# Kernel tuning notes

Measured on AMD Instinct MI355X. Metric: run time of the kernel, lower is better.

## Reference

```python
import jax, jax.numpy as jnp
import numpy as np

HIDDEN = 2048
H = 16            # num heads
Q_RANK = 1536
KV_RANK = 512
D_NOPE = 128
D_ROPE = 64
D_QK = D_NOPE + D_ROPE   # 192
D_V = 128
ROPE_BASE = 10000.0
EPS = 1e-6


def _rms_norm(x, w):
    xf = x.astype(jnp.float32)
    var = jnp.mean(xf * xf, axis=-1, keepdims=True)
    return w * (xf * jax.lax.rsqrt(var + EPS)).astype(x.dtype)


def _rotate_half(x):
    x1, x2 = x[..., : x.shape[-1] // 2], x[..., x.shape[-1] // 2:]
    return jnp.concatenate((-x2, x1), axis=-1)


def _rope_cos_sin(position_ids, dtype):
    inv_freq = 1.0 / (ROPE_BASE ** (jnp.arange(0, D_ROPE, 2, dtype=jnp.float32) / D_ROPE))
    freqs = position_ids.astype(jnp.float32)[..., None] * inv_freq  # [b,s,32]
    emb = jnp.concatenate((freqs, freqs), axis=-1)                  # [b,s,64]
    return jnp.cos(emb).astype(dtype), jnp.sin(emb).astype(dtype)


def setup_inputs() -> dict:
    key = jax.random.key(0)
    ks = jax.random.split(key, 8)
    b, s = 1, 2048
    scale = 0.02
    return {
        "hidden_states": jax.random.normal(ks[0], (b, s, HIDDEN), jnp.float32),
        "position_ids": jnp.broadcast_to(jnp.arange(s, dtype=jnp.int64)[None, :], (b, s)),
        "q_a_w": jax.random.normal(ks[1], (Q_RANK, HIDDEN), jnp.float32) * scale,
        "q_a_ln_w": jnp.ones((Q_RANK,), jnp.float32),
        "q_b_w": jax.random.normal(ks[2], (H * D_QK, Q_RANK), jnp.float32) * scale,
        "kv_a_w": jax.random.normal(ks[3], (KV_RANK + D_ROPE, HIDDEN), jnp.float32) * scale,
        "kv_a_ln_w": jnp.ones((KV_RANK,), jnp.float32),
        "kv_b_w": jax.random.normal(ks[4], (H * (D_NOPE + D_V), KV_RANK), jnp.float32) * scale,
        "o_w": jax.random.normal(ks[5], (HIDDEN, H * D_V), jnp.float32) * scale,
    }


def reference(hidden_states, position_ids, q_a_w, q_a_ln_w, q_b_w, kv_a_w, kv_a_ln_w, kv_b_w, o_w):
    b, s, _ = hidden_states.shape
    softmax_scale = D_QK ** (-0.5)

    # Q path: low-rank down-proj -> RMSNorm -> up-proj
    q_a = hidden_states @ q_a_w.T                              # [b,s,q_rank]
    q = (_rms_norm(q_a, q_a_ln_w) @ q_b_w.T).reshape(b, s, H, D_QK)
    q_nope, q_pe = q[..., :D_NOPE], q[..., D_NOPE:]

    # KV path: joint down-proj -> split latent / rope part
    kv_a = hidden_states @ kv_a_w.T                            # [b,s,kv_rank+rope]
    compressed_kv = _rms_norm(kv_a[..., :KV_RANK], kv_a_ln_w)  # [b,s,kv_rank]
    k_pe = kv_a[..., KV_RANK:]                                 # [b,s,rope]
    kv_b = (compressed_kv @ kv_b_w.T).reshape(b, s, H, D_NOPE + D_V)
    k_nope, v = kv_b[..., :D_NOPE], kv_b[..., D_NOPE:]

    # decoupled RoPE on the rope slice
    cos, sin = _rope_cos_sin(position_ids, hidden_states.dtype)  # [b,s,64]
    cos, sin = cos[:, :, None, :], sin[:, :, None, :]            # [b,s,1,64]
    q_pe = q_pe * cos + _rotate_half(q_pe) * sin                 # [b,s,H,64]
    k_pe_h = jnp.broadcast_to(k_pe[:, :, None, :], (b, s, H, D_ROPE))
    k_pe_h = k_pe_h * cos + _rotate_half(k_pe_h) * sin

    q_full = jnp.concatenate([q_nope, q_pe], axis=-1)            # [b,s,H,192]
    k_full = jnp.concatenate([k_nope, k_pe_h], axis=-1)          # [b,s,H,192]

    # naive materialized attention (matches reference)
    scores = jnp.einsum("bqhd,bkhd->bhqk", q_full, k_full) * softmax_scale
    causal = jnp.triu(jnp.full((s, s), -jnp.inf, dtype=scores.dtype), k=1)
    scores = scores + causal
    probs = jax.nn.softmax(scores.astype(jnp.float32), axis=-1).astype(q_full.dtype)
    attn = jnp.einsum("bhqk,bkhd->bqhd", probs, v).reshape(b, s, H * D_V)
    return attn @ o_w.T
```

## Files before the change

### kernel.cpp

```cpp
#include <hip/hip_runtime.h>
#include <stdint.h>

#define S_LEN 2048
#define HIDDEN_ 2048
#define NH 16
#define QR 1536
#define KVR 512
#define DN 128
#define DR 64
#define DQK 192
#define DV 128
#define NQKV 2112

#define KT_STRIDE 6144
#define VT_STRIDE 4096

typedef __attribute__((ext_vector_type(8))) short bf16x8;
typedef __attribute__((ext_vector_type(4))) float f32x4;
typedef __attribute__((ext_vector_type(4))) unsigned short u16x4;
typedef unsigned short u16;
typedef unsigned int u32;

#define GLOAD_LDS16(g, l)                                                      \
    __builtin_amdgcn_global_load_lds(                                          \
        (const __attribute__((address_space(1))) void*)(g),                    \
        (__attribute__((address_space(3))) void*)(l), 16, 0, 0)

__device__ inline float bf2f(u16 x) {
    union { u32 u; float f; } v; v.u = ((u32)x) << 16; return v.f;
}
__device__ inline u16 f2bf(float f) {
    union { float f; u32 u; } v; v.f = f;
    u32 u = v.u;
    return (u16)((u + 0x7fffu + ((u >> 16) & 1u)) >> 16);
}

__global__ void cvt_multi(const float* s0, u16* d0, int n0,
                          const float* s1, u16* d1, int n1,
                          const float* s2, u16* d2, int n2,
                          const float* s3, u16* d3, int n3,
                          const float* s4, u16* d4, int n4,
                          const float* s5, u16* d5, int n5)
{
    const float* src; u16* dst; int n;
    switch (blockIdx.y) {
        case 0: src = s0; dst = d0; n = n0; break;
        case 1: src = s1; dst = d1; n = n1; break;
        case 2: src = s2; dst = d2; n = n2; break;
        case 3: src = s3; dst = d3; n = n3; break;
        case 4: src = s4; dst = d4; n = n4; break;
        default: src = s5; dst = d5; n = n5; break;
    }
    int i = (blockIdx.x * 256 + threadIdx.x) * 4;
    if (i + 3 < n) {
        float4 v = *(const float4*)(src + i);
        u16x4 o;
        o[0] = f2bf(v.x); o[1] = f2bf(v.y); o[2] = f2bf(v.z); o[3] = f2bf(v.w);
        *(u16x4*)(dst + i) = o;
    }
}

__device__ __forceinline__
void gemm_body(const u16* __restrict__ A, const u16* __restrict__ B,
               void* __restrict__ Cv, int M, int N, int Kloop, int ld,
               int out_f32, int bx, int by)
{
    __shared__ u16 sA[128 * 32];
    __shared__ u16 sB[128 * 32];
    const int tid  = threadIdx.x;
    const int wave = tid >> 6;
    const int lane = tid & 63;
    const int l16  = lane & 15;
    const int quad = lane >> 4;
    const int m_blk = by * 128;
    const int n_blk = bx * 128;
    const int wm = (wave >> 1) * 64;
    const int wn = (wave & 1) * 64;

    const f32x4 zero4 = {0.f, 0.f, 0.f, 0.f};
    f32x4 acc[4][4];
#pragma unroll
    for (int i = 0; i < 4; i++)
#pragma unroll
        for (int j = 0; j < 4; j++) acc[i][j] = zero4;

    const int srow = lane >> 2;
    const int scol = (lane & 3) * 8;

    for (int k0 = 0; k0 < Kloop; k0 += 32) {
        __syncthreads();
#pragma unroll
        for (int p = 0; p < 2; p++) {
            const int rbase = wave * 32 + p * 16;
            const int row = rbase + srow;
            const u16* ga = A + (size_t)(m_blk + row) * ld + k0 + scol;
            GLOAD_LDS16(ga, &sA[rbase * 32]);
            int brow = n_blk + row; if (brow >= N) brow = N - 1;
            const u16* gb = B + (size_t)brow * ld + k0 + scol;
            GLOAD_LDS16(gb, &sB[rbase * 32]);
        }
        __syncthreads();

        bf16x8 af[4], bfr[4];
#pragma unroll
        for (int i = 0; i < 4; i++)
            af[i] = *(const bf16x8*)(sA + (wm + i * 16 + l16) * 32 + quad * 8);
#pragma unroll
        for (int j = 0; j < 4; j++)
            bfr[j] = *(const bf16x8*)(sB + (wn + j * 16 + l16) * 32 + quad * 8);
#pragma unroll
        for (int i = 0; i < 4; i++)
#pragma unroll
            for (int j = 0; j < 4; j++)
                acc[i][j] = __builtin_amdgcn_mfma_f32_16x16x32_bf16(
                    af[i], bfr[j], acc[i][j], 0, 0, 0);
    }

#pragma unroll
    for (int i = 0; i < 4; i++)
#pragma unroll
        for (int j = 0; j < 4; j++)
#pragma unroll
            for (int r = 0; r < 4; r++) {
                int mrow = m_blk + wm + i * 16 + quad * 4 + r;
                int ncol = n_blk + wn + j * 16 + l16;
                if (ncol < N) {
                    if (out_f32)
                        ((float*)Cv)[(size_t)mrow * N + ncol] = acc[i][j][r];
                    else
                        ((u16*)Cv)[(size_t)mrow * N + ncol] = f2bf(acc[i][j][r]);
                }
            }
}

__global__ __launch_bounds__(256, 3)
void gemm_splitk(const u16* __restrict__ A, const u16* __restrict__ B,
                 float* __restrict__ C0, float* __restrict__ C1,
                 int M, int N, int Kh, int ld)
{
    float* C = blockIdx.z ? C1 : C0;
    gemm_body(A + (size_t)blockIdx.z * Kh, B + (size_t)blockIdx.z * Kh,
              C, M, N, Kh, ld, 1, blockIdx.x, blockIdx.y);
}

__global__ __launch_bounds__(256, 3)
void gemm_dual(const u16* A0, const u16* B0, u16* C0, int M0, int N0, int K0,
               const u16* A1, const u16* B1, u16* C1, int M1, int N1, int K1)
{
    if (blockIdx.z == 0) {
        if ((int)blockIdx.x >= (N0 + 127) / 128) return;
        gemm_body(A0, B0, C0, M0, N0, K0, K0, 0, blockIdx.x, blockIdx.y);
    } else {
        gemm_body(A1, B1, C1, M1, N1, K1, K1, 0, blockIdx.x, blockIdx.y);
    }
}

__global__ void rmsnorm2_k(const float* __restrict__ P0, const float* __restrict__ P1,
                           const float* __restrict__ W0, u16* __restrict__ Y0,
                           const float* __restrict__ W1, u16* __restrict__ Y1,
                           u16* __restrict__ kpe)
{
    const int row = blockIdx.x;
    const float* p0 = P0 + (size_t)row * NQKV;
    const float* p1 = P1 + (size_t)row * NQKV;
    __shared__ float xbuf[QR];
    __shared__ float red[4];
    int off, len; const float* W; u16* Y;
    if (blockIdx.y == 0) { off = 0;  len = QR;  W = W0; Y = Y0 + (size_t)row * QR;  }
    else                 { off = QR; len = KVR; W = W1; Y = Y1 + (size_t)row * KVR; }
    float ss = 0.f;
    for (int i = threadIdx.x; i < len; i += 256) {
        float v = p0[off + i] + p1[off + i];
        xbuf[i] = v;
        ss += v * v;
    }
#pragma unroll
    for (int o = 32; o; o >>= 1) ss += __shfl_down(ss, o, 64);
    if ((threadIdx.x & 63) == 0) red[threadIdx.x >> 6] = ss;
    __syncthreads();
    float tot = red[0] + red[1] + red[2] + red[3];
    float inv = 1.0f / sqrtf(tot / (float)len + 1e-6f);
    for (int i = threadIdx.x; i < len; i += 256)
        Y[i] = f2bf(W[i] * xbuf[i] * inv);
    if (blockIdx.y == 1 && threadIdx.x < DR) {
        int i = threadIdx.x;
        kpe[(size_t)row * DR + i] = f2bf(p0[QR + KVR + i] + p1[QR + KVR + i]);
    }
}

__global__ void rope_repack(const u16* __restrict__ q,
                            const u16* __restrict__ kvb,
                            const u16* __restrict__ kpe_b,
                            u16* __restrict__ Q, u16* __restrict__ Kf)
{
    const int s = blockIdx.x;
    const float pos = (float)s;
    const int t = threadIdx.x;
    __shared__ float cs[64], sn[64];
    __shared__ u16 kpe_r[64];
    if (t < 64) {
        int jf = t & 31;
        float freq = powf(10000.f, -(float)(2 * jf) / 64.f);
        float ang = pos * freq;
        cs[t] = cosf(ang);
        sn[t] = sinf(ang);
    }
    __syncthreads();
    if (t < 64) {
        int j = t;
        float x = bf2f(kpe_b[(size_t)s * DR + j]);
        float other = (j < 32) ? -bf2f(kpe_b[(size_t)s * DR + j + 32])
                               :  bf2f(kpe_b[(size_t)s * DR + j - 32]);
        kpe_r[j] = f2bf(x * cs[j] + other * sn[j]);
    }
    __syncthreads();

    for (int idx = t; idx < NH * 24; idx += 256) {
        const int h  = idx / 24;
        const int cg = idx % 24;
        const int d0v = cg * 8;
        const size_t qbase = (size_t)s * (NH * DQK) + h * DQK;
        bf16x8 qv, kv;
        if (d0v < DN) {
            qv = *(const bf16x8*)(q + qbase + d0v);
            kv = *(const bf16x8*)(kvb + (size_t)s * (NH * 256) + h * 256 + d0v);
        } else {
            const int j0 = d0v - DN;
#pragma unroll
            for (int e = 0; e < 8; e++) {
                int j = j0 + e;
                float x = bf2f(q[qbase + DN + j]);
                float other = (j < 32) ? -bf2f(q[qbase + DN + j + 32])
                                       :  bf2f(q[qbase + DN + j - 32]);
                qv[e] = (short)f2bf(x * cs[j] + other * sn[j]);
                kv[e] = (short)kpe_r[j];
            }
        }
        *(bf16x8*)&Q[((size_t)h * S_LEN + s) * DQK + d0v] = qv;
        const size_t koff = (size_t)(h * 64 + (s >> 5)) * KT_STRIDE
                          + (size_t)(cg * 32 + (s & 31)) * 8;
        *(bf16x8*)&Kf[koff] = kv;
    }
}

__global__ void transpose_v(const u16* __restrict__ kvb, u16* __restrict__ Vt)
{
    __shared__ u16 tile[64][72];
    const int h  = blockIdx.z;
    const int s0 = blockIdx.x * 64;
    const int d0 = blockIdx.y * 64;
    const int t  = threadIdx.x;
#pragma unroll
    for (int p = 0; p < 2; p++) {
        int c = p * 256 + t;
        int r = c >> 3, col = (c & 7) * 8;
        *(bf16x8*)&tile[r][col] =
            *(const bf16x8*)&kvb[(size_t)(s0 + r) * (NH * 256) + h * 256 + 128 + d0 + col];
    }
    __syncthreads();
#pragma unroll
    for (int p = 0; p < 2; p++) {
        int c = p * 256 + t;
        int dr = c >> 3, sc = (c & 7) * 8;
        bf16x8 v;
#pragma unroll
        for (int j = 0; j < 8; j++) v[j] = (short)tile[sc + j][dr];
        const int s_abs   = s0 + sc;
        const int kt      = s_abs >> 5;
        const int schunk  = (s_abs & 31) >> 3;
        const size_t voff = (size_t)(h * 64 + kt) * VT_STRIDE
                          + (size_t)(schunk * 128 + (d0 + dr)) * 8;
        *(bf16x8*)&Vt[voff] = v;
    }
}

__global__ __launch_bounds__(256, 3)
void mla_attn(const u16* __restrict__ Q, const u16* __restrict__ Kf,
              const u16* __restrict__ Vt, u16* __restrict__ attn,
              float* __restrict__ part)
{
    const int lin = blockIdx.x + 48 * blockIdx.y;
    const int h   = ((lin & 7) << 1) | ((lin >> 3) & 1);
    const int bx  = lin >> 4;

    int s, tb, te, cIdx; bool direct;
    if (bx < 16)      { s = 16 + bx; tb = 0;  te = 32;        cIdx = 0; direct = false; }
    else if (bx < 32) { s = 47 - bx; tb = 32; te = 2 * s + 2; cIdx = 1; direct = false; }
    else              { s = 47 - bx; tb = 0;  te = 2 * s + 2; cIdx = 0; direct = true;  }

    const int wave  = threadIdx.x >> 6;
    const int lane  = threadIdx.x & 63;
    const int l16   = lane & 15;
    const int quad  = lane >> 4;
    const int q0    = s * 64 + wave * 16;
    const int qrow  = q0 + l16;

    const u16* Qh  = Q  + (size_t)h * S_LEN * DQK;
    const u16* Kh  = Kf + (size_t)h * 64 * KT_STRIDE;
    const u16* Vth = Vt + (size_t)h * 64 * VT_STRIDE;

    __shared__ u16 sK[2][24 * 32 * 8];
    __shared__ u16 sV[2][4 * 128 * 8];
    __shared__ u16 pbuf[4][16][36];
    u16 (*pb)[36] = pbuf[wave];

    bf16x8 qf[6];
#pragma unroll
    for (int st = 0; st < 6; st++)
        qf[st] = *(const bf16x8*)(Qh + (size_t)qrow * DQK + st * 32 + quad * 8);

    const f32x4 zero4 = {0.f, 0.f, 0.f, 0.f};
    f32x4 oacc[8];
#pragma unroll
    for (int t = 0; t < 8; t++) oacc[t] = zero4;
    float mrow = -INFINITY, lrow = 0.f;

    const float scale = 0.07216878364870323f;

    auto stage = [&](int buf, int kt) {
        const u16* kp = Kh + (size_t)kt * KT_STRIDE;
#pragma unroll
        for (int g = 0; g < 3; g++)
            GLOAD_LDS16(kp + (g * 256 + wave * 64 + lane) * 8,
                        &sK[buf][(g * 256 + wave * 64) * 8]);
        const u16* vp = Vth + (size_t)kt * VT_STRIDE;
#pragma unroll
        for (int g = 0; g < 2; g++)
            GLOAD_LDS16(vp + (g * 256 + wave * 64 + lane) * 8,
                        &sV[buf][(g * 256 + wave * 64) * 8]);
    };

    stage(0, tb);

    for (int kt = tb; kt < te; kt++) {
        const int c0  = kt * 32;
        const int cur = (kt - tb) & 1;
        __syncthreads();
        if (kt + 1 < te) stage(cur ^ 1, kt + 1);

        if (c0 <= q0 + 15) {
            f32x4 s0 = zero4, s1 = zero4;
            __builtin_amdgcn_s_setprio(1);
#pragma unroll
            for (int st = 0; st < 6; st++) {
                bf16x8 k0 = *(const bf16x8*)&sK[cur][((st * 4 + quad) * 32 + l16) * 8];
                bf16x8 k1 = *(const bf16x8*)&sK[cur][((st * 4 + quad) * 32 + 16 + l16) * 8];
                s0 = __builtin_amdgcn_mfma_f32_16x16x32_bf16(k0, qf[st], s0, 0, 0, 0);
                s1 = __builtin_amdgcn_mfma_f32_16x16x32_bf16(k1, qf[st], s1, 0, 0, 0);
            }
            __builtin_amdgcn_s_setprio(0);
            bf16x8 vfr[8];
#pragma unroll
            for (int t = 0; t < 8; t++)
                vfr[t] = *(const bf16x8*)&sV[cur][(quad * 128 + t * 16 + l16) * 8];

            const bool full = (c0 + 31 <= q0);
            float v0[4], v1[4];
#pragma unroll
            for (int r = 0; r < 4; r++) {
                v0[r] = s0[r] * scale;
                v1[r] = s1[r] * scale;
                if (!full) {
                    if (c0 + quad * 4 + r > qrow)      v0[r] = -INFINITY;
                    if (c0 + 16 + quad * 4 + r > qrow) v1[r] = -INFINITY;
                }
            }
            float lm = fmaxf(fmaxf(fmaxf(v0[0], v0[1]), fmaxf(v0[2], v0[3])),
                             fmaxf(fmaxf(v1[0], v1[1]), fmaxf(v1[2], v1[3])));
            lm = fmaxf(lm, __shfl_xor(lm, 16, 64));
            lm = fmaxf(lm, __shfl_xor(lm, 32, 64));

            float mref;
            if (__all(lm <= mrow + 8.f)) {
                mref = mrow;
            } else {
                mref = fmaxf(mrow, lm);
                const float alpha = __expf(mrow - mref);
#pragma unroll
                for (int t = 0; t < 8; t++) oacc[t] *= alpha;
                lrow *= alpha;
                mrow = mref;
            }

            float p0[4], p1[4], rs = 0.f;
#pragma unroll
            for (int r = 0; r < 4; r++) {
                p0[r] = __expf(v0[r] - mref);
                p1[r] = __expf(v1[r] - mref);
                rs += p0[r] + p1[r];
            }
            rs += __shfl_xor(rs, 16, 64);
            rs += __shfl_xor(rs, 32, 64);
            lrow += rs;

            u16x4 pk0, pk1;
#pragma unroll
            for (int r = 0; r < 4; r++) { pk0[r] = f2bf(p0[r]); pk1[r] = f2bf(p1[r]); }
            *(u16x4*)&pb[l16][quad * 4]      = pk0;
            *(u16x4*)&pb[l16][16 + quad * 4] = pk1;
            asm volatile("s_waitcnt lgkmcnt(0)" ::: "memory");
            bf16x8 pfrag = *(const bf16x8*)(&pb[l16][quad * 8]);

            __builtin_amdgcn_s_setprio(1);
#pragma unroll
            for (int t = 0; t < 8; t++)
                oacc[t] = __builtin_amdgcn_mfma_f32_16x16x32_bf16(vfr[t], pfrag,
                                                                  oacc[t], 0, 0, 0);
            __builtin_amdgcn_s_setprio(0);
        }
    }

    if (direct) {
        const float linv = 1.0f / lrow;
#pragma unroll
        for (int t = 0; t < 8; t++) {
            u16x4 ov;
#pragma unroll
            for (int r = 0; r < 4; r++) ov[r] = f2bf(oacc[t][r] * linv);
            *(u16x4*)&attn[(size_t)qrow * (NH * DV) + h * DV + t * 16 + quad * 4] = ov;
        }
    } else {
        float* pout = part + ((size_t)(h * 16 + (s - 16)) * 2 + cIdx) * 8320;
        const int rowl = wave * 16 + l16;
#pragma unroll
        for (int t = 0; t < 8; t++) {
            float4 ov = {oacc[t][0], oacc[t][1], oacc[t][2], oacc[t][3]};
            *(float4*)&pout[(size_t)rowl * 128 + t * 16 + quad * 4] = ov;
        }
        if (quad == 0) {
            pout[8192 + rowl] = mrow;
            pout[8256 + rowl] = lrow;
        }
    }
}

__global__ void attn_combine(const float* __restrict__ part, u16* __restrict__ attn)
{
    const int h = blockIdx.y, sIdx = blockIdx.x;
    const int s = 16 + sIdx;
    const float* p0 = part + ((size_t)(h * 16 + sIdx) * 2 + 0) * 8320;
    const float* p1 = p0 + 8320;
    for (int e = threadIdx.x; e < 8192; e += 256) {
        int row = e >> 7, d = e & 127;
        float m0 = p0[8192 + row], m1 = p1[8192 + row];
        float l0 = p0[8256 + row], l1 = p1[8256 + row];
        float M  = fmaxf(m0, m1);
        float w0 = __expf(m0 - M), w1 = __expf(m1 - M);
        float o  = (w0 * p0[e] + w1 * p1[e]) / (w0 * l0 + w1 * l1);
        attn[(size_t)(s * 64 + row) * (NH * DV) + h * DV + d] = f2bf(o);
    }
}

__global__ void addf2(const float* __restrict__ a, const float* __restrict__ b,
                      float* __restrict__ o, int n)
{
    int i = (blockIdx.x * 256 + threadIdx.x) * 4;
    if (i + 3 < n) {
        float4 va = *(const float4*)(a + i);
        float4 vb = *(const float4*)(b + i);
        float4 vo = {va.x + vb.x, va.y + vb.y, va.z + vb.z, va.w + vb.w};
        *(float4*)(o + i) = vo;
    }
}

extern "C" void kernel_launch(void* const* d_in, const int* in_sizes, int n_in,
                              void* d_out, int out_size, void* d_ws, size_t ws_size,
                              hipStream_t stream)
{
    const float* hid      = (const float*)d_in[0];
    const float* q_a_w    = (const float*)d_in[2];
    const float* q_a_ln_w = (const float*)d_in[3];
    const float* q_b_w    = (const float*)d_in[4];
    const float* kv_a_w   = (const float*)d_in[5];
    const float* kv_a_ln_w= (const float*)d_in[6];
    const float* kv_b_w   = (const float*)d_in[7];
    const float* o_w      = (const float*)d_in[8];

    char* base = (char*)d_ws;
    u16* qkvaw_b = (u16*)(base + 0);
    u16* qbw_b   = (u16*)(base + 8650752);
    u16* kvbw_b  = (u16*)(base + 18087936);
    u16* ow_b    = (u16*)(base + 22282240);
    u16* hid_b   = (u16*)(base + 30670848);
    float* P0    = (float*)(base + 39059456);
    float* P1    = (float*)(base + 56360960);
    u16* q_n     = (u16*)(base + 73662464);
    u16* ckv     = (u16*)(base + 79953920);
    u16* kpe_b   = (u16*)(base + 82051072);
    u16* qb      = (u16*)(base + 82313216);
    u16* kvb     = (u16*)(base + 94896128);
    u16* Qb      = (u16*)(base + 39059456);
    u16* Kb      = (u16*)(base + 51642368);
    u16* Vtb     = (u16*)(base + 64225280);
    u16* attnb   = (u16*)(base + 72613888);
    float* partb = (float*)(base + 94896128);
    float* PO0   = (float*)(base + 82313216);
    float* PO1   = (float*)(base + 99090432);

    cvt_multi<<<dim3(4608, 6), 256, 0, stream>>>(
        hid,    hid_b,                          HIDDEN_ * S_LEN,
        q_a_w,  qkvaw_b,                        QR * HIDDEN_,
        kv_a_w, qkvaw_b + (size_t)QR * HIDDEN_, (KVR + DR) * HIDDEN_,
        q_b_w,  qbw_b,                          NH * DQK * QR,
        kv_b_w, kvbw_b,                         NH * 256 * KVR,
        o_w,    ow_b,                           HIDDEN_ * NH * DV);

    gemm_splitk<<<dim3((NQKV + 127) / 128, S_LEN / 128, 2), 256, 0, stream>>>(
        hid_b, qkvaw_b, P0, P1, S_LEN, NQKV, HIDDEN_ / 2, HIDDEN_);
    rmsnorm2_k<<<dim3(S_LEN, 2), 256, 0, stream>>>(
        P0, P1, q_a_ln_w, q_n, kv_a_ln_w, ckv, kpe_b);
    gemm_dual<<<dim3(32, S_LEN / 128, 2), 256, 0, stream>>>(
        q_n, qbw_b, qb,  S_LEN, NH * DQK, QR,
        ckv, kvbw_b, kvb, S_LEN, NH * 256, KVR);
    rope_repack<<<S_LEN, 256, 0, stream>>>(qb, kvb, kpe_b, Qb, Kb);
    transpose_v<<<dim3(S_LEN / 64, DV / 64, NH), 256, 0, stream>>>(kvb, Vtb);
    mla_attn<<<dim3(48, NH), 256, 0, stream>>>(Qb, Kb, Vtb, attnb, partb);
    attn_combine<<<dim3(16, NH), 256, 0, stream>>>(partb, attnb);
    gemm_splitk<<<dim3(HIDDEN_ / 128, S_LEN / 128, 2), 256, 0, stream>>>(
        attnb, ow_b, PO0, PO1, S_LEN, HIDDEN_, HIDDEN_ / 2, HIDDEN_);
    addf2<<<dim3((S_LEN * HIDDEN_) / 1024), 256, 0, stream>>>(
        PO0, PO1, (float*)d_out, S_LEN * HIDDEN_);
}
```

Measured before the change: 344.3 us.

## Fold softmax scale into Q, use exp2, and swap the LDS P transpose for bpermute

The softmax scale times log2(e) is folded into Q during rope_repack, so the attention loop drops its per-score multiply and uses the native exp2 intrinsic, with the rescale threshold adjusted to match. The per-wave LDS round trip that converted P into an MFMA operand is replaced by ds_bpermute lane shuffles, removing the shared buffer and its waitcnt. The per-tile cross-lane row-sum reduction is deferred to a single reduction after the loop. The index order of the second-half split blocks is also reversed to change scheduling and load balance. Scaling Q before rounding to bf16 changes its rounding slightly.

```diff
diff --git a/kernel.cpp b/kernel.cpp
--- a/kernel.cpp
+++ b/kernel.cpp
@@ -193,6 +193,7 @@
                             const u16* __restrict__ kpe_b,
                             u16* __restrict__ Q, u16* __restrict__ Kf)
 {
+    const float QSC = 0.07216878364870323f * 1.4426950408889634f;
     const int s = blockIdx.x;
     const float pos = (float)s;
     const int t = threadIdx.x;
@@ -222,7 +223,10 @@
         const size_t qbase = (size_t)s * (NH * DQK) + h * DQK;
         bf16x8 qv, kv;
         if (d0v < DN) {
-            qv = *(const bf16x8*)(q + qbase + d0v);
+            bf16x8 qr = *(const bf16x8*)(q + qbase + d0v);
+#pragma unroll
+            for (int e = 0; e < 8; e++)
+                qv[e] = (short)f2bf(bf2f((u16)qr[e]) * QSC);
             kv = *(const bf16x8*)(kvb + (size_t)s * (NH * 256) + h * 256 + d0v);
         } else {
             const int j0 = d0v - DN;
@@ -232,7 +236,7 @@
                 float x = bf2f(q[qbase + DN + j]);
                 float other = (j < 32) ? -bf2f(q[qbase + DN + j + 32])
                                        :  bf2f(q[qbase + DN + j - 32]);
-                qv[e] = (short)f2bf(x * cs[j] + other * sn[j]);
+                qv[e] = (short)f2bf((x * cs[j] + other * sn[j]) * QSC);
                 kv[e] = (short)kpe_r[j];
             }
         }
@@ -285,7 +289,7 @@
 
     int s, tb, te, cIdx; bool direct;
     if (bx < 16)      { s = 16 + bx; tb = 0;  te = 32;        cIdx = 0; direct = false; }
-    else if (bx < 32) { s = 47 - bx; tb = 32; te = 2 * s + 2; cIdx = 1; direct = false; }
+    else if (bx < 32) { s = bx;      tb = 32; te = 2 * s + 2; cIdx = 1; direct = false; }
     else              { s = 47 - bx; tb = 0;  te = 2 * s + 2; cIdx = 0; direct = true;  }
 
     const int wave  = threadIdx.x >> 6;
@@ -301,8 +305,6 @@
 
     __shared__ u16 sK[2][24 * 32 * 8];
     __shared__ u16 sV[2][4 * 128 * 8];
-    __shared__ u16 pbuf[4][16][36];
-    u16 (*pb)[36] = pbuf[wave];
 
     bf16x8 qf[6];
 #pragma unroll
@@ -314,8 +316,6 @@
 #pragma unroll
     for (int t = 0; t < 8; t++) oacc[t] = zero4;
     float mrow = -INFINITY, lrow = 0.f;
-
-    const float scale = 0.07216878364870323f;
 
     auto stage = [&](int buf, int kt) {
         const u16* kp = Kh + (size_t)kt * KT_STRIDE;
@@ -358,8 +358,8 @@
             float v0[4], v1[4];
 #pragma unroll
             for (int r = 0; r < 4; r++) {
-                v0[r] = s0[r] * scale;
-                v1[r] = s1[r] * scale;
+                v0[r] = s0[r];
+                v1[r] = s1[r];
                 if (!full) {
                     if (c0 + quad * 4 + r > qrow)      v0[r] = -INFINITY;
                     if (c0 + 16 + quad * 4 + r > qrow) v1[r] = -INFINITY;
@@ -371,11 +371,11 @@
             lm = fmaxf(lm, __shfl_xor(lm, 32, 64));
 
             float mref;
-            if (__all(lm <= mrow + 8.f)) {
+            if (__all(lm <= mrow + 11.5416f)) {
                 mref = mrow;
             } else {
                 mref = fmaxf(mrow, lm);
-                const float alpha = __expf(mrow - mref);
+                const float alpha = __builtin_amdgcn_exp2f(mrow - mref);
 #pragma unroll
                 for (int t = 0; t < 8; t++) oacc[t] *= alpha;
                 lrow *= alpha;
@@ -385,21 +385,33 @@
             float p0[4], p1[4], rs = 0.f;
 #pragma unroll
             for (int r = 0; r < 4; r++) {
-                p0[r] = __expf(v0[r] - mref);
-                p1[r] = __expf(v1[r] - mref);
+                p0[r] = __builtin_amdgcn_exp2f(v0[r] - mref);
+                p1[r] = __builtin_amdgcn_exp2f(v1[r] - mref);
                 rs += p0[r] + p1[r];
             }
-            rs += __shfl_xor(rs, 16, 64);
-            rs += __shfl_xor(rs, 32, 64);
             lrow += rs;
 
-            u16x4 pk0, pk1;
-#pragma unroll
-            for (int r = 0; r < 4; r++) { pk0[r] = f2bf(p0[r]); pk1[r] = f2bf(p1[r]); }
-            *(u16x4*)&pb[l16][quad * 4]      = pk0;
-            *(u16x4*)&pb[l16][16 + quad * 4] = pk1;
-            asm volatile("s_waitcnt lgkmcnt(0)" ::: "memory");
-            bf16x8 pfrag = *(const bf16x8*)(&pb[l16][quad * 8]);
+            u32 A0 = (u32)f2bf(p0[0]) | ((u32)f2bf(p0[1]) << 16);
+            u32 A1 = (u32)f2bf(p0[2]) | ((u32)f2bf(p0[3]) << 16);
+            u32 B0 = (u32)f2bf(p1[0]) | ((u32)f2bf(p1[1]) << 16);
+            u32 B1 = (u32)f2bf(p1[2]) | ((u32)f2bf(p1[3]) << 16);
+            const int a0 = (((quad & 1) << 5) + l16) << 2;
+            const int a1 = a0 + 64;
+            u32 Y0 = (u32)__builtin_amdgcn_ds_bpermute(a0, (int)A0);
+            u32 Y1 = (u32)__builtin_amdgcn_ds_bpermute(a0, (int)A1);
+            u32 Y2 = (u32)__builtin_amdgcn_ds_bpermute(a1, (int)A0);
+            u32 Y3 = (u32)__builtin_amdgcn_ds_bpermute(a1, (int)A1);
+            u32 Z0 = (u32)__builtin_amdgcn_ds_bpermute(a0, (int)B0);
+            u32 Z1 = (u32)__builtin_amdgcn_ds_bpermute(a0, (int)B1);
+            u32 Z2 = (u32)__builtin_amdgcn_ds_bpermute(a1, (int)B0);
+            u32 Z3 = (u32)__builtin_amdgcn_ds_bpermute(a1, (int)B1);
+            const bool useA = quad < 2;
+            union { u32 w[4]; bf16x8 v; } pf;
+            pf.w[0] = useA ? Y0 : Z0;
+            pf.w[1] = useA ? Y1 : Z1;
+            pf.w[2] = useA ? Y2 : Z2;
+            pf.w[3] = useA ? Y3 : Z3;
+            bf16x8 pfrag = pf.v;
 
             __builtin_amdgcn_s_setprio(1);
 #pragma unroll
@@ -410,8 +422,12 @@
         }
     }
 
+    float lsum = lrow;
+    lsum += __shfl_xor(lsum, 16, 64);
+    lsum += __shfl_xor(lsum, 32, 64);
+
     if (direct) {
-        const float linv = 1.0f / lrow;
+        const float linv = 1.0f / lsum;
 #pragma unroll
         for (int t = 0; t < 8; t++) {
             u16x4 ov;
@@ -429,7 +445,7 @@
         }
         if (quad == 0) {
             pout[8192 + rowl] = mrow;
-            pout[8256 + rowl] = lrow;
+            pout[8256 + rowl] = lsum;
         }
     }
 }
@@ -445,7 +461,8 @@
         float m0 = p0[8192 + row], m1 = p1[8192 + row];
         float l0 = p0[8256 + row], l1 = p1[8256 + row];
         float M  = fmaxf(m0, m1);
-        float w0 = __expf(m0 - M), w1 = __expf(m1 - M);
+        float w0 = __builtin_amdgcn_exp2f(m0 - M);
+        float w1 = __builtin_amdgcn_exp2f(m1 - M);
         float o  = (w0 * p0[e] + w1 * p1[e]) / (w0 * l0 + w1 * l1);
         attn[(size_t)(s * 64 + row) * (NH * DV) + h * DV + d] = f2bf(o);
     }
```

After: 336.0 us. 2.4% less time.
